# Optimization experiments

Hardware: AMD Instinct MI355X
Metric: run time of the kernel (lower is better)

## Reference

```python
import jax, jax.numpy as jnp
import numpy as np

B = 8192          # batch_size
NB = 4096         # num_banks (== mask length)
PAD = NB // 2     # reflect pad on each side


def setup_inputs() -> dict:
    key = jax.random.key(0)
    k1, k2, k3 = jax.random.split(key, 3)
    logits = jax.random.normal(k1, (NB,), dtype=jnp.float32) * 0.1
    u = jax.random.uniform(k2, (B, NB), dtype=jnp.float32)          # Bernoulli uniforms
    shift = jax.random.randint(k3, (B,), 0, NB, dtype=jnp.int32)    # per-sample shift
    return {"logits": logits, "u": u, "shift": shift}


def reference(logits, u, shift):
    # Bernoulli(sigmoid(logits)) sample via inverse-CDF on externally supplied uniforms
    p = jax.nn.sigmoid(logits)                       # (NB,)
    grid = (u < p).astype(jnp.float32)               # (B, NB)
    # Bernoulli log_prob summed over banks: g*log(p) + (1-g)*log(1-p)
    log_probs = (grid * jax.nn.log_sigmoid(logits)
                 + (1.0 - grid) * jax.nn.log_sigmoid(-logits)).sum(axis=1)  # (B,)
    # reflect-pad along bank axis, then gather a shifted window of length NB
    padded = jnp.pad(grid, ((0, 0), (PAD, PAD)), mode="reflect")    # (B, NB+2*PAD)
    idx = shift[:, None].astype(jnp.int32) + jnp.arange(NB, dtype=jnp.int32)[None, :]
    masks = jnp.take_along_axis(padded, idx, axis=1)[:, None, :]    # (B, 1, NB)
    return masks, log_probs
```

## Files before the change

kernel.cpp:

```cpp
#include <hip/hip_runtime.h>
#include <math.h>

#define NB 4096
#define PAD 2048
#define BLOCK 256

__device__ __forceinline__ int mirror_idx(int i) {
    i = ::abs(i);
    return (i < NB) ? i : (2 * (NB - 1) - i);
}

__global__ void fbmp_precompute(const float* __restrict__ logits, float* __restrict__ ws) {
    int j = blockIdx.x * blockDim.x + threadIdx.x;
    if (j >= NB) return;
    float x = logits[j];
    double xd = (double)x;
    float e = (float)exp(-xd);
    float p = 1.0f / (1.0f + e);
    float lsp = (float)(-log1p(exp(-xd)));
    float lsn = (float)(-log1p(exp(xd)));
    ws[j] = p;
    ws[NB + j] = lsp;
    ws[2 * NB + j] = lsn;
}

__global__ __launch_bounds__(BLOCK) void fbmp_main(
    const float* __restrict__ u, const int* __restrict__ shift,
    const float* __restrict__ ws,
    float* __restrict__ masks, float* __restrict__ logp)
{
    __shared__ float sg[NB];
    __shared__ float sred[BLOCK / 64];

    const int b = blockIdx.x;
    const float4* __restrict__ u4   = (const float4*)(u + (size_t)b * NB);
    const float4* __restrict__ p4   = (const float4*)(ws);
    const float4* __restrict__ lsp4 = (const float4*)(ws + NB);
    const float4* __restrict__ lsn4 = (const float4*)(ws + 2 * NB);

    float acc = 0.0f;
    for (int i = threadIdx.x; i < NB / 4; i += BLOCK) {
        float4 uv = u4[i];
        float4 pv = p4[i];
        float4 ap = lsp4[i];
        float4 an = lsn4[i];
        bool c0 = uv.x < pv.x;
        bool c1 = uv.y < pv.y;
        bool c2 = uv.z < pv.z;
        bool c3 = uv.w < pv.w;
        acc += (c0 ? ap.x : an.x) + (c1 ? ap.y : an.y)
             + (c2 ? ap.z : an.z) + (c3 ? ap.w : an.w);
        float4 g;
        g.x = c0 ? 1.0f : 0.0f;
        g.y = c1 ? 1.0f : 0.0f;
        g.z = c2 ? 1.0f : 0.0f;
        g.w = c3 ? 1.0f : 0.0f;
        ((float4*)sg)[i] = g;
    }

    #pragma unroll
    for (int off = 32; off > 0; off >>= 1)
        acc += __shfl_down(acc, off, 64);
    const int lane = threadIdx.x & 63;
    const int wid  = threadIdx.x >> 6;
    if (lane == 0) sred[wid] = acc;
    __syncthreads();
    if (threadIdx.x == 0) {
        float t = 0.0f;
        #pragma unroll
        for (int w = 0; w < BLOCK / 64; ++w) t += sred[w];
        logp[b] = t;
    }

    const int s = shift[b] - PAD;
    float4* __restrict__ m4 = (float4*)(masks + (size_t)b * NB);
    for (int i = threadIdx.x; i < NB / 4; i += BLOCK) {
        int k = 4 * i + s;
        float4 o;
        o.x = sg[mirror_idx(k + 0)];
        o.y = sg[mirror_idx(k + 1)];
        o.z = sg[mirror_idx(k + 2)];
        o.w = sg[mirror_idx(k + 3)];
        m4[i] = o;
    }
}

extern "C" void kernel_launch(void* const* d_in, const int* in_sizes, int n_in,
                              void* d_out, int out_size, void* d_ws, size_t ws_size,
                              hipStream_t stream) {
    const float* logits = (const float*)d_in[0];
    const float* u      = (const float*)d_in[1];
    const int*   shift  = (const int*)d_in[2];
    const int B = in_sizes[2];

    float* ws    = (float*)d_ws;
    float* masks = (float*)d_out;
    float* logp  = (float*)d_out + (size_t)B * NB;

    fbmp_precompute<<<(NB + 255) / 256, 256, 0, stream>>>(logits, ws);
    fbmp_main<<<B, BLOCK, 0, stream>>>(u, shift, ws, masks, logp);
}
```

Measured before the change: 241.9 us.

## Gather mask directly from global u with mirrored indices, drop LDS grid buffer

The main kernel no longer builds the Bernoulli grid in shared memory. It recomputes each mask element by gathering u and p at the mirrored shifted index straight from global memory, which removes the 16KB LDS array and its bank-conflicted reads. The log-prob is rewritten as a constant sum of log_sigmoid(-x) plus a conditional sum of the difference, so each element needs three streamed loads instead of four. The precompute becomes a single block that reduces the constant. In exchange, each u row is read twice (once contiguously, once as a scalar gather that should mostly hit cache), and the summation order changes slightly.

```diff
diff --git a/kernel.cpp b/kernel.cpp
--- a/kernel.cpp
+++ b/kernel.cpp
@@ -4,6 +4,7 @@
 #define NB 4096
 #define PAD 2048
 #define BLOCK 256
+#define V4 (NB / 4 / BLOCK)
 
 __device__ __forceinline__ int mirror_idx(int i) {
     i = ::abs(i);
@@ -11,17 +12,32 @@
 }
 
 __global__ void fbmp_precompute(const float* __restrict__ logits, float* __restrict__ ws) {
-    int j = blockIdx.x * blockDim.x + threadIdx.x;
-    if (j >= NB) return;
-    float x = logits[j];
-    double xd = (double)x;
-    float e = (float)exp(-xd);
-    float p = 1.0f / (1.0f + e);
-    float lsp = (float)(-log1p(exp(-xd)));
-    float lsn = (float)(-log1p(exp(xd)));
-    ws[j] = p;
-    ws[NB + j] = lsp;
-    ws[2 * NB + j] = lsn;
+    __shared__ float sred[BLOCK / 64];
+    float lsnsum = 0.0f;
+    for (int j = threadIdx.x; j < NB; j += BLOCK) {
+        float x = logits[j];
+        double xd = (double)x;
+        float e = (float)exp(-xd);
+        float p = 1.0f / (1.0f + e);
+        float lsp = (float)(-log1p(exp(-xd)));
+        float lsn = (float)(-log1p(exp(xd)));
+        ws[j] = p;
+        ws[NB + j] = lsp - lsn;
+        lsnsum += lsn;
+    }
+    #pragma unroll
+    for (int off = 32; off > 0; off >>= 1)
+        lsnsum += __shfl_down(lsnsum, off, 64);
+    const int lane = threadIdx.x & 63;
+    const int wid  = threadIdx.x >> 6;
+    if (lane == 0) sred[wid] = lsnsum;
+    __syncthreads();
+    if (threadIdx.x == 0) {
+        float t = 0.0f;
+        #pragma unroll
+        for (int w = 0; w < BLOCK / 64; ++w) t += sred[w];
+        ws[2 * NB] = t;
+    }
 }
 
 __global__ __launch_bounds__(BLOCK) void fbmp_main(
@@ -29,59 +45,65 @@
     const float* __restrict__ ws,
     float* __restrict__ masks, float* __restrict__ logp)
 {
-    __shared__ float sg[NB];
     __shared__ float sred[BLOCK / 64];
 
     const int b = blockIdx.x;
-    const float4* __restrict__ u4   = (const float4*)(u + (size_t)b * NB);
-    const float4* __restrict__ p4   = (const float4*)(ws);
-    const float4* __restrict__ lsp4 = (const float4*)(ws + NB);
-    const float4* __restrict__ lsn4 = (const float4*)(ws + 2 * NB);
+    const int t = threadIdx.x;
+    const float* __restrict__ urow = u + (size_t)b * NB;
+    const float* __restrict__ p    = ws;
+    const float4* __restrict__ u4  = (const float4*)urow;
+    const float4* __restrict__ p4  = (const float4*)ws;
+    const float4* __restrict__ d4  = (const float4*)(ws + NB);
+    const int s = shift[b] - PAD;
+
+    float um[4 * V4];
+    float pm[4 * V4];
+    #pragma unroll
+    for (int i = 0; i < V4; ++i) {
+        #pragma unroll
+        for (int e = 0; e < 4; ++e) {
+            int k = 4 * (t + i * BLOCK) + e;
+            int j = mirror_idx(k + s);
+            um[4 * i + e] = urow[j];
+            pm[4 * i + e] = p[j];
+        }
+    }
 
     float acc = 0.0f;
-    for (int i = threadIdx.x; i < NB / 4; i += BLOCK) {
-        float4 uv = u4[i];
-        float4 pv = p4[i];
-        float4 ap = lsp4[i];
-        float4 an = lsn4[i];
-        bool c0 = uv.x < pv.x;
-        bool c1 = uv.y < pv.y;
-        bool c2 = uv.z < pv.z;
-        bool c3 = uv.w < pv.w;
-        acc += (c0 ? ap.x : an.x) + (c1 ? ap.y : an.y)
-             + (c2 ? ap.z : an.z) + (c3 ? ap.w : an.w);
-        float4 g;
-        g.x = c0 ? 1.0f : 0.0f;
-        g.y = c1 ? 1.0f : 0.0f;
-        g.z = c2 ? 1.0f : 0.0f;
-        g.w = c3 ? 1.0f : 0.0f;
-        ((float4*)sg)[i] = g;
+    #pragma unroll
+    for (int i = 0; i < V4; ++i) {
+        float4 uv = u4[t + i * BLOCK];
+        float4 pv = p4[t + i * BLOCK];
+        float4 dv = d4[t + i * BLOCK];
+        acc += (uv.x < pv.x ? dv.x : 0.0f)
+             + (uv.y < pv.y ? dv.y : 0.0f)
+             + (uv.z < pv.z ? dv.z : 0.0f)
+             + (uv.w < pv.w ? dv.w : 0.0f);
+    }
+
+    float4* __restrict__ m4 = (float4*)(masks + (size_t)b * NB);
+    #pragma unroll
+    for (int i = 0; i < V4; ++i) {
+        float4 o;
+        o.x = (um[4 * i + 0] < pm[4 * i + 0]) ? 1.0f : 0.0f;
+        o.y = (um[4 * i + 1] < pm[4 * i + 1]) ? 1.0f : 0.0f;
+        o.z = (um[4 * i + 2] < pm[4 * i + 2]) ? 1.0f : 0.0f;
+        o.w = (um[4 * i + 3] < pm[4 * i + 3]) ? 1.0f : 0.0f;
+        m4[t + i * BLOCK] = o;
     }
 
     #pragma unroll
     for (int off = 32; off > 0; off >>= 1)
         acc += __shfl_down(acc, off, 64);
-    const int lane = threadIdx.x & 63;
-    const int wid  = threadIdx.x >> 6;
+    const int lane = t & 63;
+    const int wid  = t >> 6;
     if (lane == 0) sred[wid] = acc;
     __syncthreads();
-    if (threadIdx.x == 0) {
-        float t = 0.0f;
+    if (t == 0) {
+        float tot = 0.0f;
         #pragma unroll
-        for (int w = 0; w < BLOCK / 64; ++w) t += sred[w];
-        logp[b] = t;
-    }
-
-    const int s = shift[b] - PAD;
-    float4* __restrict__ m4 = (float4*)(masks + (size_t)b * NB);
-    for (int i = threadIdx.x; i < NB / 4; i += BLOCK) {
-        int k = 4 * i + s;
-        float4 o;
-        o.x = sg[mirror_idx(k + 0)];
-        o.y = sg[mirror_idx(k + 1)];
-        o.z = sg[mirror_idx(k + 2)];
-        o.w = sg[mirror_idx(k + 3)];
-        m4[i] = o;
+        for (int w = 0; w < BLOCK / 64; ++w) tot += sred[w];
+        logp[b] = tot + ws[2 * NB];
     }
 }
 
@@ -97,6 +119,6 @@
     float* masks = (float*)d_out;
     float* logp  = (float*)d_out + (size_t)B * NB;
 
-    fbmp_precompute<<<(NB + 255) / 256, 256, 0, stream>>>(logits, ws);
+    fbmp_precompute<<<1, BLOCK, 0, stream>>>(logits, ws);
     fbmp_main<<<B, BLOCK, 0, stream>>>(u, shift, ws, masks, logp);
 }
```

New measurement: 297.7 us. +23.0%, slower.
